# Optimization experiments

Hardware: AMD Instinct MI355X
Metric: run time of the kernel (lower is better)

## Reference

```python
import jax, jax.numpy as jnp
import numpy as np

B, F_DIM, C, M = 16, 64, 64, 512
OUT_CH = 32
DT = 1.0


def setup_inputs() -> dict:
    key = jax.random.key(0)
    ks = jax.random.split(key, 8)
    x = jax.random.normal(ks[0], (B, F_DIM, C, M), dtype=jnp.float32)
    A = jax.random.uniform(ks[1], (B, M, C, C), dtype=jnp.float32)
    phys_prior = jax.random.normal(ks[2], (B, C, M), dtype=jnp.float32)
    kappa = jnp.array(0.1, dtype=jnp.float32)
    alpha = jnp.array(0.05, dtype=jnp.float32)
    # r_phi MLP: Linear(1,16) -> ELU -> Linear(16,1)
    w1 = jax.random.normal(ks[3], (16, 1), dtype=jnp.float32) * 1.0
    b1 = jnp.zeros((16,), dtype=jnp.float32)
    w2 = jax.random.normal(ks[4], (1, 16), dtype=jnp.float32) * 0.25
    b2 = jnp.zeros((1,), dtype=jnp.float32)
    # 1x1 Conv2d(1, OUT_CH): weight (OUT_CH,1,1,1) -> flatten to (OUT_CH,)
    pw = jax.random.normal(ks[5], (OUT_CH,), dtype=jnp.float32)
    pb = jnp.zeros((OUT_CH,), dtype=jnp.float32)
    return {"x": x, "A": A, "phys_prior": phys_prior, "kappa": kappa,
            "alpha": alpha, "w1": w1, "b1": b1, "w2": w2, "b2": b2,
            "pw": pw, "pb": pb}


def reference(x, A, phys_prior, kappa, alpha, w1, b1, w2, b2, pw, pb):
    # x: (B,F,C,M), A: (B,M,C,C), phys_prior: (B,C,M)
    s = x.mean(axis=1)                      # (B,C,M)
    deg = A.sum(axis=-1)                    # (B,M,C)
    sT = jnp.transpose(s, (0, 2, 1))        # (B,M,C)
    # torch einsum 'bmcd,bmcn->bmdn' with n=1 contracts over c: (A^T s)
    As = jnp.einsum('bmcd,bmc->bmd', A, sT)  # (B,M,C)
    Ls = jnp.transpose(deg * sT - As, (0, 2, 1))  # (B,C,M)
    k = jax.nn.softplus(kappa)
    # tiny MLP on per-(b,c) mean over M
    r_in = s.mean(axis=-1, keepdims=True)   # (B,C,1)
    h = jax.nn.elu(r_in @ w1.T + b1)        # (B,C,16)
    r = h @ w2.T + b2                       # (B,C,1), broadcasts over M
    phys_corr = alpha * phys_prior          # (B,C,M)
    s_new = s - DT * k * Ls + DT * (r + phys_corr)  # (B,C,M)
    # 1x1 conv over (B,1,C,M): pointwise scale+bias per output channel
    corr = s_new[:, None, :, :] * pw[None, :, None, None] + pb[None, :, None, None]
    return corr  # (B,OUT_CH,C,M)
```

## Files before the change

### kernel.cpp

```cpp
#include <hip/hip_runtime.h>
#include <math.h>

#define B_  16
#define F_  64
#define C_  64
#define M_  512
#define OC_ 32

__global__ __launch_bounds__(128, 6) void k1_mean(
    const float* __restrict__ x,
    float* __restrict__ s_out, float* __restrict__ rpart)
{
    const int gid = blockIdx.x;
    const int q   = gid & 3;
    const int bc  = gid >> 2;
    const int b   = bc >> 6;
    const int c   = bc & 63;
    const int t   = threadIdx.x;
    const int tf  = t >> 5;
    const int tm  = t & 31;
    const int m4  = (q << 5) + tm;

    const size_t rowbase = ((size_t)b * F_ * C_ + c) * M_;
    float ax = 0.f, ay = 0.f, az = 0.f, aw = 0.f;
    #pragma unroll 8
    for (int j = 0; j < 16; ++j) {
        const int f = (tf << 4) + j;
        const float4 v = ((const float4*)(x + rowbase + (size_t)f * C_ * M_))[m4];
        ax += v.x; ay += v.y; az += v.z; aw += v.w;
    }

    __shared__ float4 red[4][32];
    red[tf][tm] = make_float4(ax, ay, az, aw);
    __syncthreads();

    if (tf == 0) {
        const float4 r1 = red[1][tm], r2 = red[2][tm], r3 = red[3][tm];
        const float inv_f = 1.0f / (float)F_;
        float4 sv;
        sv.x = (ax + r1.x + r2.x + r3.x) * inv_f;
        sv.y = (ay + r1.y + r2.y + r3.y) * inv_f;
        sv.z = (az + r1.z + r2.z + r3.z) * inv_f;
        sv.w = (aw + r1.w + r2.w + r3.w) * inv_f;
        ((float4*)(s_out + (size_t)bc * M_))[m4] = sv;

        float p = sv.x + sv.y + sv.z + sv.w;
        #pragma unroll
        for (int off = 16; off > 0; off >>= 1) p += __shfl_xor(p, off);
        if (t == 0) rpart[gid] = p;
    }
}

__global__ __launch_bounds__(256, 4) void k2_laplace(
    const float* __restrict__ A, const float* __restrict__ phys,
    const float* __restrict__ kappa_p, const float* __restrict__ alpha_p,
    const float* __restrict__ s_in, const float* __restrict__ rpart,
    const float* __restrict__ w1, const float* __restrict__ b1,
    const float* __restrict__ w2, const float* __restrict__ b2,
    float* __restrict__ snew)
{
    __shared__ float s_l[C_ * 5];
    __shared__ float ph_l[C_ * 5];
    __shared__ float sn_l[C_ * 5];
    __shared__ float r_l[C_];

    const int blk = blockIdx.x;
    const int b   = blk >> 7;
    const int m0  = (blk & 127) << 2;
    const int t   = threadIdx.x;

    if (t < 64) {
        const float4 sv = *(const float4*)(s_in + ((size_t)(b * C_ + t)) * M_ + m0);
        s_l[t*5+0] = sv.x; s_l[t*5+1] = sv.y; s_l[t*5+2] = sv.z; s_l[t*5+3] = sv.w;
    } else if (t < 128) {
        const int tt = t - 64;
        const float4 pv = *(const float4*)(phys + ((size_t)(b * C_ + tt)) * M_ + m0);
        ph_l[tt*5+0] = pv.x; ph_l[tt*5+1] = pv.y; ph_l[tt*5+2] = pv.z; ph_l[tt*5+3] = pv.w;
    } else if (t < 192) {
        const int tt = t - 128;
        const float4 rp = ((const float4*)rpart)[b * C_ + tt];
        const float rin = (rp.x + rp.y + rp.z + rp.w) * (1.0f / (float)M_);
        float r = b2[0];
        #pragma unroll
        for (int j = 0; j < 16; ++j) {
            float hh = rin * w1[j] + b1[j];
            hh = (hh > 0.f) ? hh : (expf(hh) - 1.f);
            r += hh * w2[j];
        }
        r_l[tt] = r;
    }
    __syncthreads();

    const int w = t >> 6;
    const int l = t & 63;
    const int g = l >> 4;
    const int h = l & 15;

    const float4* Ap = (const float4*)(A + ((size_t)(b * M_ + m0 + w)) * (C_ * C_));
    float4 v[16];
    #pragma unroll
    for (int j = 0; j < 16; ++j) v[j] = Ap[j * 64 + l];

    float d[16];
    float a0 = 0.f, a1 = 0.f, a2 = 0.f, a3 = 0.f;
    #pragma unroll
    for (int j = 0; j < 16; ++j) {
        const float sr = s_l[(4*j + g) * 5 + w];
        d[j] = v[j].x + v[j].y + v[j].z + v[j].w;
        a0 += sr * v[j].x; a1 += sr * v[j].y;
        a2 += sr * v[j].z; a3 += sr * v[j].w;
    }

    float e[8];
    #pragma unroll
    for (int jj = 0; jj < 8; ++jj) {
        const float sd = (h & 8) ? d[jj] : d[jj + 8];
        const float rv = __shfl_xor(sd, 8);
        e[jj] = ((h & 8) ? d[jj + 8] : d[jj]) + rv;
    }
    float f2[4];
    #pragma unroll
    for (int jj = 0; jj < 4; ++jj) {
        const float sd = (h & 4) ? e[jj] : e[jj + 4];
        const float rv = __shfl_xor(sd, 4);
        f2[jj] = ((h & 4) ? e[jj + 4] : e[jj]) + rv;
    }
    float g2[2];
    #pragma unroll
    for (int jj = 0; jj < 2; ++jj) {
        const float sd = (h & 2) ? f2[jj] : f2[jj + 2];
        const float rv = __shfl_xor(sd, 2);
        g2[jj] = ((h & 2) ? f2[jj + 2] : f2[jj]) + rv;
    }
    float deg;
    {
        const float sd = (h & 1) ? g2[0] : g2[1];
        const float rv = __shfl_xor(sd, 1);
        deg = ((h & 1) ? g2[1] : g2[0]) + rv;
    }

    const float send0 = (g & 1) ? a0 : a1;
    const float send1 = (g & 1) ? a2 : a3;
    const float r0 = __shfl_xor(send0, 16);
    const float r1 = __shfl_xor(send1, 16);
    const float b0v = ((g & 1) ? a1 : a0) + r0;
    const float b1v = ((g & 1) ? a3 : a2) + r1;
    const float send2 = (g & 2) ? b0v : b1v;
    const float r2 = __shfl_xor(send2, 32);
    const float Asv = ((g & 2) ? b1v : b0v) + r2;

    const float kk = log1pf(expf(kappa_p[0]));
    const float al = alpha_p[0];
    const int   i  = 4 * h + g;
    const float sval = s_l[i * 5 + w];
    const float Ls   = deg * sval - Asv;
    sn_l[i * 5 + w]  = sval - kk * Ls + (r_l[i] + al * ph_l[i * 5 + w]);
    __syncthreads();

    if (t < 64) {
        float4 ov;
        ov.x = sn_l[t*5+0]; ov.y = sn_l[t*5+1];
        ov.z = sn_l[t*5+2]; ov.w = sn_l[t*5+3];
        *(float4*)(snew + ((size_t)(b * C_ + t)) * M_ + m0) = ov;
    }
}

__global__ __launch_bounds__(256) void k3_expand(
    const float* __restrict__ snew,
    const float* __restrict__ pw, const float* __restrict__ pb,
    float* __restrict__ out)
{
    const int n4 = (B_ * OC_ * C_ * M_) / 4;
    for (int i = blockIdx.x * blockDim.x + threadIdx.x; i < n4;
         i += gridDim.x * blockDim.x) {
        const int m4 = i & 127;
        const int c  = (i >> 7) & 63;
        const int o  = (i >> 13) & 31;
        const int b  = i >> 18;
        const float4 v = ((const float4*)snew)[(((b << 6) + c) << 7) + m4];
        const float w  = pw[o];
        const float bb = pb[o];
        float4 r;
        r.x = v.x * w + bb; r.y = v.y * w + bb;
        r.z = v.z * w + bb; r.w = v.w * w + bb;
        ((float4*)out)[i] = r;
    }
}

extern "C" void kernel_launch(void* const* d_in, const int* in_sizes, int n_in,
                              void* d_out, int out_size, void* d_ws, size_t ws_size,
                              hipStream_t stream)
{
    const float* x     = (const float*)d_in[0];
    const float* A     = (const float*)d_in[1];
    const float* phys  = (const float*)d_in[2];
    const float* kappa = (const float*)d_in[3];
    const float* alpha = (const float*)d_in[4];
    const float* w1    = (const float*)d_in[5];
    const float* b1    = (const float*)d_in[6];
    const float* w2    = (const float*)d_in[7];
    const float* b2    = (const float*)d_in[8];
    const float* pw    = (const float*)d_in[9];
    const float* pb    = (const float*)d_in[10];
    float* out = (float*)d_out;

    float* ws    = (float*)d_ws;
    float* s     = ws;
    float* snew  = ws + (size_t)B_ * C_ * M_;
    float* rpart = ws + (size_t)2 * B_ * C_ * M_;

    k1_mean<<<B_ * C_ * 4, 128, 0, stream>>>(x, s, rpart);
    k2_laplace<<<B_ * (M_ / 4), 256, 0, stream>>>(A, phys, kappa, alpha, s, rpart,
                                                  w1, b1, w2, b2, snew);
    k3_expand<<<2048, 256, 0, stream>>>(snew, pw, pb, out);
}
```

Measured before the change: 77.55 us.

## Give each wave four A tiles with double-buffered register prefetch in Laplacian kernel

The Laplacian kernel now has each wavefront process four consecutive m positions instead of one, with A tiles loaded into two register buffers so the next tile's loads overlap the current tile's reduction. The block-wide shared staging of the result and the block-level r-MLP split are gone. Each lane computes its own output channel directly and writes a float4, and the MLP result is broadcast with a shuffle. Grid size drops from 2048 to 512 blocks and launch bounds go to 2 blocks per CU. This trades occupancy and register pressure (32 float4 live) for memory-level parallelism per wave and fewer syncs.

```diff
diff --git a/kernel.cpp b/kernel.cpp
--- a/kernel.cpp
+++ b/kernel.cpp
@@ -51,61 +51,16 @@
     }
 }
 
-__global__ __launch_bounds__(256, 4) void k2_laplace(
-    const float* __restrict__ A, const float* __restrict__ phys,
-    const float* __restrict__ kappa_p, const float* __restrict__ alpha_p,
-    const float* __restrict__ s_in, const float* __restrict__ rpart,
-    const float* __restrict__ w1, const float* __restrict__ b1,
-    const float* __restrict__ w2, const float* __restrict__ b2,
-    float* __restrict__ snew)
-{
-    __shared__ float s_l[C_ * 5];
-    __shared__ float ph_l[C_ * 5];
-    __shared__ float sn_l[C_ * 5];
-    __shared__ float r_l[C_];
-
-    const int blk = blockIdx.x;
-    const int b   = blk >> 7;
-    const int m0  = (blk & 127) << 2;
-    const int t   = threadIdx.x;
-
-    if (t < 64) {
-        const float4 sv = *(const float4*)(s_in + ((size_t)(b * C_ + t)) * M_ + m0);
-        s_l[t*5+0] = sv.x; s_l[t*5+1] = sv.y; s_l[t*5+2] = sv.z; s_l[t*5+3] = sv.w;
-    } else if (t < 128) {
-        const int tt = t - 64;
-        const float4 pv = *(const float4*)(phys + ((size_t)(b * C_ + tt)) * M_ + m0);
-        ph_l[tt*5+0] = pv.x; ph_l[tt*5+1] = pv.y; ph_l[tt*5+2] = pv.z; ph_l[tt*5+3] = pv.w;
-    } else if (t < 192) {
-        const int tt = t - 128;
-        const float4 rp = ((const float4*)rpart)[b * C_ + tt];
-        const float rin = (rp.x + rp.y + rp.z + rp.w) * (1.0f / (float)M_);
-        float r = b2[0];
-        #pragma unroll
-        for (int j = 0; j < 16; ++j) {
-            float hh = rin * w1[j] + b1[j];
-            hh = (hh > 0.f) ? hh : (expf(hh) - 1.f);
-            r += hh * w2[j];
-        }
-        r_l[tt] = r;
-    }
-    __syncthreads();
-
-    const int w = t >> 6;
-    const int l = t & 63;
-    const int g = l >> 4;
-    const int h = l & 15;
-
-    const float4* Ap = (const float4*)(A + ((size_t)(b * M_ + m0 + w)) * (C_ * C_));
-    float4 v[16];
-    #pragma unroll
-    for (int j = 0; j < 16; ++j) v[j] = Ap[j * 64 + l];
-
+struct DegAs { float deg, As; };
+
+__device__ __forceinline__ DegAs reduce_tile(
+    const float4 (&v)[16], const float* SLw, int mi, int g, int h)
+{
     float d[16];
     float a0 = 0.f, a1 = 0.f, a2 = 0.f, a3 = 0.f;
     #pragma unroll
     for (int j = 0; j < 16; ++j) {
-        const float sr = s_l[(4*j + g) * 5 + w];
+        const float sr = SLw[(4 * j + g) * 5 + mi];
         d[j] = v[j].x + v[j].y + v[j].z + v[j].w;
         a0 += sr * v[j].x; a1 += sr * v[j].y;
         a2 += sr * v[j].z; a3 += sr * v[j].w;
@@ -149,20 +104,78 @@
     const float r2 = __shfl_xor(send2, 32);
     const float Asv = ((g & 2) ? b1v : b0v) + r2;
 
+    DegAs out; out.deg = deg; out.As = Asv;
+    return out;
+}
+
+__global__ __launch_bounds__(256, 2) void k2_stream(
+    const float* __restrict__ A, const float* __restrict__ phys,
+    const float* __restrict__ kappa_p, const float* __restrict__ alpha_p,
+    const float* __restrict__ s_in, const float* __restrict__ rpart,
+    const float* __restrict__ w1, const float* __restrict__ b1,
+    const float* __restrict__ w2, const float* __restrict__ b2,
+    float* __restrict__ snew)
+{
+    __shared__ float SL[4 * C_ * 5];
+
+    const int t  = threadIdx.x;
+    const int w  = t >> 6;
+    const int l  = t & 63;
+    const int wg = blockIdx.x * 4 + w;
+    const int b  = wg >> 7;
+    const int m0 = (wg & 127) << 2;
+    const int g  = l >> 4;
+    const int h  = l & 15;
+    const int i  = 4 * h + g;
+
+    float* SLw = &SL[w * (C_ * 5)];
+
+    {
+        const float4 sc = *(const float4*)(s_in + ((size_t)(b * C_ + l)) * M_ + m0);
+        SLw[l * 5 + 0] = sc.x; SLw[l * 5 + 1] = sc.y;
+        SLw[l * 5 + 2] = sc.z; SLw[l * 5 + 3] = sc.w;
+    }
+    const float4 sv4 = *(const float4*)(s_in + ((size_t)(b * C_ + i)) * M_ + m0);
+    const float4 pv4 = *(const float4*)(phys + ((size_t)(b * C_ + i)) * M_ + m0);
+    float r_i;
+    {
+        const float4 rp = ((const float4*)rpart)[b * C_ + l];
+        const float rin = (rp.x + rp.y + rp.z + rp.w) * (1.0f / (float)M_);
+        float r = b2[0];
+        #pragma unroll
+        for (int j = 0; j < 16; ++j) {
+            float hh = rin * w1[j] + b1[j];
+            hh = (hh > 0.f) ? hh : (expf(hh) - 1.f);
+            r += hh * w2[j];
+        }
+        r_i = __shfl(r, i, 64);
+    }
     const float kk = log1pf(expf(kappa_p[0]));
     const float al = alpha_p[0];
-    const int   i  = 4 * h + g;
-    const float sval = s_l[i * 5 + w];
-    const float Ls   = deg * sval - Asv;
-    sn_l[i * 5 + w]  = sval - kk * Ls + (r_l[i] + al * ph_l[i * 5 + w]);
     __syncthreads();
 
-    if (t < 64) {
-        float4 ov;
-        ov.x = sn_l[t*5+0]; ov.y = sn_l[t*5+1];
-        ov.z = sn_l[t*5+2]; ov.w = sn_l[t*5+3];
-        *(float4*)(snew + ((size_t)(b * C_ + t)) * M_ + m0) = ov;
-    }
+    const float* Abase = A + ((size_t)(b * M_ + m0)) * (C_ * C_);
+    float4 vA[16], vB[16];
+    #pragma unroll
+    for (int j = 0; j < 16; ++j) vA[j] = ((const float4*)(Abase))[j * 64 + l];
+    #pragma unroll
+    for (int j = 0; j < 16; ++j) vB[j] = ((const float4*)(Abase + 4096))[j * 64 + l];
+
+    const DegAs da0 = reduce_tile(vA, SLw, 0, g, h);
+    #pragma unroll
+    for (int j = 0; j < 16; ++j) vA[j] = ((const float4*)(Abase + 8192))[j * 64 + l];
+    const DegAs da1 = reduce_tile(vB, SLw, 1, g, h);
+    #pragma unroll
+    for (int j = 0; j < 16; ++j) vB[j] = ((const float4*)(Abase + 12288))[j * 64 + l];
+    const DegAs da2 = reduce_tile(vA, SLw, 2, g, h);
+    const DegAs da3 = reduce_tile(vB, SLw, 3, g, h);
+
+    float4 ov;
+    ov.x = sv4.x - kk * (da0.deg * sv4.x - da0.As) + (r_i + al * pv4.x);
+    ov.y = sv4.y - kk * (da1.deg * sv4.y - da1.As) + (r_i + al * pv4.y);
+    ov.z = sv4.z - kk * (da2.deg * sv4.z - da2.As) + (r_i + al * pv4.z);
+    ov.w = sv4.w - kk * (da3.deg * sv4.w - da3.As) + (r_i + al * pv4.w);
+    *(float4*)(snew + ((size_t)(b * C_ + i)) * M_ + m0) = ov;
 }
 
 __global__ __launch_bounds__(256) void k3_expand(
@@ -210,7 +223,7 @@
     float* rpart = ws + (size_t)2 * B_ * C_ * M_;
 
     k1_mean<<<B_ * C_ * 4, 128, 0, stream>>>(x, s, rpart);
-    k2_laplace<<<B_ * (M_ / 4), 256, 0, stream>>>(A, phys, kappa, alpha, s, rpart,
-                                                  w1, b1, w2, b2, snew);
+    k2_stream<<<512, 256, 0, stream>>>(A, phys, kappa, alpha, s, rpart,
+                                       w1, b1, w2, b2, snew);
     k3_expand<<<2048, 256, 0, stream>>>(snew, pw, pb, out);
 }
```

New measurement: 77.19 us. About the same (-0.5%).
